# Kernel tuning notes

Hardware: AMD Instinct MI355X
Metric: run time of the kernel (lower is better)

## Reference

```python
import jax, jax.numpy as jnp
import numpy as np

B, N, HIDDEN, IN_DIM = 4, 1024, 64, 6


def setup_inputs() -> dict:
    key = jax.random.key(0)
    ks = jax.random.split(key, 8)
    pos = jax.random.normal(ks[0], (B, N, 3), dtype=jnp.float32)
    vel = jax.random.normal(ks[1], (B, N, 3), dtype=jnp.float32)
    # edge MLP params (Linear stores W as [out,in] in torch; we use [in,out])
    s1 = 1.0 / np.sqrt(IN_DIM)
    s2 = 1.0 / np.sqrt(HIDDEN)
    W1 = jax.random.uniform(ks[2], (IN_DIM, HIDDEN), jnp.float32, -s1, s1)
    b1 = jax.random.uniform(ks[3], (HIDDEN,), jnp.float32, -s1, s1)
    W2 = jax.random.uniform(ks[4], (HIDDEN, HIDDEN), jnp.float32, -s2, s2)
    b2 = jax.random.uniform(ks[5], (HIDDEN,), jnp.float32, -s2, s2)
    W3 = jax.random.uniform(ks[6], (HIDDEN, 3), jnp.float32, -s2, s2)
    b3 = jax.random.uniform(ks[7], (3,), jnp.float32, -s2, s2)
    return {"pos": pos, "vel": vel, "W1": W1, "b1": b1, "W2": W2, "b2": b2, "W3": W3, "b3": b3}


def reference(pos, vel, W1, b1, W2, b2, W3, b3):
    # all-pairs differences: r_ij[b,i,j] = pos[b,j] - pos[b,i]   [B,N,N,3]
    r_ij = pos[:, None, :, :] - pos[:, :, None, :]
    v_ij = vel[:, None, :, :] - vel[:, :, None, :]
    edge_inputs = jnp.concatenate([r_ij, v_ij], axis=-1)  # [B,N,N,6]
    h = jax.nn.relu(jnp.einsum('bijk,kh->bijh', edge_inputs, W1) + b1)
    h = jax.nn.relu(jnp.einsum('bijh,hg->bijg', h, W2) + b2)
    f_ij = jnp.einsum('bijg,go->bijo', h, W3) + b3  # [B,N,N,3]
    # antisymmetrize over (i,j); diagonal becomes exactly 0
    f_sym = (f_ij - jnp.swapaxes(f_ij, 1, 2)) * 0.5
    acc = jnp.sum(f_sym, axis=2)  # [B,N,3]
    return acc
```

## Files before the change

### kernel.cpp

```cpp
#include <hip/hip_runtime.h>

#define NB   4
#define NPTS 1024
#define HID  64
#define NU   1056

typedef float f32x4 __attribute__((ext_vector_type(4)));
typedef float f32x2 __attribute__((ext_vector_type(2)));
typedef short bf16x8 __attribute__((ext_vector_type(8)));
typedef unsigned int u32;
typedef unsigned short u16;

__device__ inline u16 f2bf(float x) {
    union { float f; unsigned u; } v; v.f = x;
    return (u16)((v.u + 0x7FFFu + ((v.u >> 16) & 1u)) >> 16);
}
__device__ inline u32 cvt_pk_bf16(float lo, float hi) {
    u32 r; asm("v_cvt_pk_bf16_f32 %0, %1, %2" : "=v"(r) : "v"(lo), "v"(hi)); return r;
}
__device__ inline u32 pk_relu2(u32 a) {
    u32 r; asm("v_pk_max_i16 %0, %1, 0" : "=v"(r) : "v"(a)); return r;
}

__global__ __launch_bounds__(256) void precompute(
    const float* __restrict__ pos, const float* __restrict__ vel,
    const float* __restrict__ W1, const float* __restrict__ W2,
    float* __restrict__ P, u16* __restrict__ W2T) {
    if (blockIdx.x == NB * NPTS / 4) {
        for (int e = threadIdx.x; e < HID * HID; e += 256) {
            const int ch = e >> 6, k = e & 63;
            W2T[e] = f2bf(W2[k * HID + ch]);
        }
        return;
    }
    const int t   = blockIdx.x * 256 + threadIdx.x;
    const int row = t >> 6;
    const int k   = t & 63;
    const float* pp = pos + row * 3;
    const float* vv = vel + row * 3;
    float acc = 0.f;
    #pragma unroll
    for (int c = 0; c < 3; ++c) acc = fmaf(pp[c], W1[c * HID + k], acc);
    #pragma unroll
    for (int c = 0; c < 3; ++c) acc = fmaf(vv[c], W1[(3 + c) * HID + k], acc);
    P[row * HID + k] = acc;
}

__device__ inline void emit_tile(const f32x4 Ht[4], float sgn, int rowbase,
                                 const float* __restrict__ W3,
                                 float* __restrict__ F, int c, int g) {
    #pragma unroll
    for (int r = 0; r < 4; ++r) {
        float f0 = 0.f, f1 = 0.f, f2 = 0.f;
        #pragma unroll
        for (int n = 0; n < 4; ++n) {
            const int ch = n * 16 + c;
            const float h = Ht[n][r];
            f0 = fmaf(h, W3[ch * 3 + 0], f0);
            f1 = fmaf(h, W3[ch * 3 + 1], f1);
            f2 = fmaf(h, W3[ch * 3 + 2], f2);
        }
        #pragma unroll
        for (int off = 1; off < 16; off <<= 1) {
            f0 += __shfl_xor(f0, off, 64);
            f1 += __shfl_xor(f1, off, 64);
            f2 += __shfl_xor(f2, off, 64);
        }
        if (c < 3) {
            const float v = (c == 0) ? f0 : ((c == 1) ? f1 : f2);
            atomicAdd(&F[(size_t)(rowbase + g * 4 + r) * 3 + c], sgn * v);
        }
    }
}

__device__ inline void do_jt(const f32x2* __restrict__ pj2,
                             const f32x2* __restrict__ bb2,
                             const f32x2* __restrict__ pi2,
                             const bf16x8* __restrict__ BfL,
                             const float* __restrict__ b2v,
                             bool accHj, f32x4* __restrict__ Hj,
                             float* __restrict__ qout) {
    union { bf16x8 v; u32 u[4]; } ap[2], am[2];
    #pragma unroll
    for (int kk = 0; kk < 2; ++kk)
        #pragma unroll
        for (int d = 0; d < 4; ++d) {
            f32x2 u  = pi2[kk * 4 + d] - pj2[kk * 4 + d];
            f32x2 tp = bb2[kk * 4 + d] - u;
            f32x2 tm = bb2[kk * 4 + d] + u;
            ap[kk].u[d] = pk_relu2(cvt_pk_bf16(tp.x, tp.y));
            am[kk].u[d] = pk_relu2(cvt_pk_bf16(tm.x, tm.y));
        }
    const f32x2 z2 = {0.f, 0.f};
    #pragma unroll
    for (int n = 0; n < 4; ++n) {
        const bf16x8 B0 = BfL[n * 64];
        const bf16x8 B1 = BfL[(4 + n) * 64];
        const f32x4 Ci = {b2v[n], b2v[n], b2v[n], b2v[n]};
        f32x4 Cp = __builtin_amdgcn_mfma_f32_16x16x32_bf16(ap[0].v, B0, Ci, 0, 0, 0);
        Cp       = __builtin_amdgcn_mfma_f32_16x16x32_bf16(ap[1].v, B1, Cp, 0, 0, 0);
        f32x4 Cm = __builtin_amdgcn_mfma_f32_16x16x32_bf16(am[0].v, B0, Ci, 0, 0, 0);
        Cm       = __builtin_amdgcn_mfma_f32_16x16x32_bf16(am[1].v, B1, Cm, 0, 0, 0);
        f32x2 cp01 = {Cp[0], Cp[1]}, cp23 = {Cp[2], Cp[3]};
        f32x2 cm01 = {Cm[0], Cm[1]}, cm23 = {Cm[2], Cm[3]};
        f32x2 d01 = __builtin_elementwise_max(cp01, z2) -
                    __builtin_elementwise_max(cm01, z2);
        f32x2 d23 = __builtin_elementwise_max(cp23, z2) -
                    __builtin_elementwise_max(cm23, z2);
        if (accHj) {
            f32x4 dd4 = {d01.x, d01.y, d23.x, d23.y};
            Hj[n] += dd4;
        }
        f32x2 q = d01 + d23;
        qout[n] = q.x + q.y;
    }
}

__global__ __launch_bounds__(128, 2) void inet_pair(
    const float* __restrict__ P,  const float* __restrict__ b1,
    const u16* __restrict__ W2T,  const float* __restrict__ b2,
    const float* __restrict__ W3, float* __restrict__ F) {
    __shared__ __align__(16) u16 sBf[512 * 8];

    const int tid = threadIdx.x;
    for (int s = tid; s < 512; s += 128) {
        const int f = s >> 6, l = s & 63;
        const int n = f & 3, kk = f >> 2, cc = l & 15, gg = l >> 4;
        ((uint4*)sBf)[s] = *(const uint4*)(W2T + (size_t)(n * 16 + cc) * HID + kk * 32 + gg * 8);
    }
    __syncthreads();

    const int lane = tid & 63;
    const int c    = lane & 15;
    const int g    = lane >> 4;
    const bf16x8* BfL = ((const bf16x8*)sBf) + lane;

    const int unit = blockIdx.x * 2 + (tid >> 6);
    const int b    = unit / NU;
    const int u    = unit - b * NU;
    int m = (int)((sqrtf((float)(4 * u + 1)) - 1.0f) * 0.5f);
    while (m * (m + 1) > u) --m;
    while ((m + 1) * (m + 2) <= u) ++m;
    const int I  = u - m * (m + 1);
    const int J0 = 2 * m, J1 = 2 * m + 1;
    const bool jt0act = (I != J1);
    const bool diag0  = (I == J0);
    const bool diag1  = (I == J1);

    const float* Pb   = P + (size_t)b * NPTS * HID;
    const int    koff = g * 8;

    union V4 { f32x4 v; f32x2 p[2]; };

    f32x2 bb2[8], pj0[8], pj1[8];
    {
        V4 v0, v1, v2, v3;
        v0.v = *(const f32x4*)(b1 + koff);
        v1.v = *(const f32x4*)(b1 + koff + 4);
        v2.v = *(const f32x4*)(b1 + koff + 32);
        v3.v = *(const f32x4*)(b1 + koff + 36);
        bb2[0] = v0.p[0]; bb2[1] = v0.p[1]; bb2[2] = v1.p[0]; bb2[3] = v1.p[1];
        bb2[4] = v2.p[0]; bb2[5] = v2.p[1]; bb2[6] = v3.p[0]; bb2[7] = v3.p[1];
    }
    {
        const float* base = Pb + (size_t)(J0 * 16 + c) * HID + koff;
        V4 v0, v1, v2, v3;
        v0.v = *(const f32x4*)(base);
        v1.v = *(const f32x4*)(base + 4);
        v2.v = *(const f32x4*)(base + 32);
        v3.v = *(const f32x4*)(base + 36);
        pj0[0] = v0.p[0]; pj0[1] = v0.p[1]; pj0[2] = v1.p[0]; pj0[3] = v1.p[1];
        pj0[4] = v2.p[0]; pj0[5] = v2.p[1]; pj0[6] = v3.p[0]; pj0[7] = v3.p[1];
    }
    {
        const float* base = Pb + (size_t)(J1 * 16 + c) * HID + koff;
        V4 v0, v1, v2, v3;
        v0.v = *(const f32x4*)(base);
        v1.v = *(const f32x4*)(base + 4);
        v2.v = *(const f32x4*)(base + 32);
        v3.v = *(const f32x4*)(base + 36);
        pj1[0] = v0.p[0]; pj1[1] = v0.p[1]; pj1[2] = v1.p[0]; pj1[3] = v1.p[1];
        pj1[4] = v2.p[0]; pj1[5] = v2.p[1]; pj1[6] = v3.p[0]; pj1[7] = v3.p[1];
    }
    float b2v[4];
    #pragma unroll
    for (int n = 0; n < 4; ++n) b2v[n] = b2[n * 16 + c];

    f32x4 Hi[4], Hj0[4], Hj1[4];
    #pragma unroll
    for (int n = 0; n < 4; ++n) {
        Hi[n]  = (f32x4){0.f, 0.f, 0.f, 0.f};
        Hj0[n] = (f32x4){0.f, 0.f, 0.f, 0.f};
        Hj1[n] = (f32x4){0.f, 0.f, 0.f, 0.f};
    }

    const float* Pi0 = Pb + (size_t)(I * 16) * HID + koff;

    for (int i1 = 0; i1 < 4; ++i1) {
        const float selm = (g == i1) ? 1.0f : 0.0f;
        #pragma unroll
        for (int i2 = 0; i2 < 4; ++i2) {
            const float* pib = Pi0 + (size_t)(i1 * 4 + i2) * HID;
            V4 w0, w1, w2, w3;
            w0.v = *(const f32x4*)(pib);
            w1.v = *(const f32x4*)(pib + 4);
            w2.v = *(const f32x4*)(pib + 32);
            w3.v = *(const f32x4*)(pib + 36);
            f32x2 pi2[8];
            pi2[0] = w0.p[0]; pi2[1] = w0.p[1]; pi2[2] = w1.p[0]; pi2[3] = w1.p[1];
            pi2[4] = w2.p[0]; pi2[5] = w2.p[1]; pi2[6] = w3.p[0]; pi2[7] = w3.p[1];

            float q0[4], q1[4];
            if (jt0act) {
                do_jt(pj0, bb2, pi2, BfL, b2v, !diag0, Hj0, q0);
            } else {
                q0[0] = q0[1] = q0[2] = q0[3] = 0.f;
            }
            do_jt(pj1, bb2, pi2, BfL, b2v, !diag1, Hj1, q1);

            #pragma unroll
            for (int n = 0; n < 4; ++n) {
                float s = q0[n] + q1[n];
                s += __shfl_xor(s, 16, 64);
                s += __shfl_xor(s, 32, 64);
                Hi[n][i2] = fmaf(selm, s, Hi[n][i2]);
            }
        }
    }

    const int rowbase = b * NPTS;
    emit_tile(Hi, 0.5f, rowbase + I * 16, W3, F, c, g);
    if (jt0act && !diag0)
        emit_tile(Hj0, -0.5f, rowbase + J0 * 16, W3, F, c, g);
    if (!diag1)
        emit_tile(Hj1, -0.5f, rowbase + J1 * 16, W3, F, c, g);
}

extern "C" void kernel_launch(void* const* d_in, const int* in_sizes, int n_in,
                              void* d_out, int out_size, void* d_ws, size_t ws_size,
                              hipStream_t stream) {
    const float* pos = (const float*)d_in[0];
    const float* vel = (const float*)d_in[1];
    const float* W1  = (const float*)d_in[2];
    const float* b1  = (const float*)d_in[3];
    const float* W2  = (const float*)d_in[4];
    const float* b2  = (const float*)d_in[5];
    const float* W3  = (const float*)d_in[6];
    const float* b3  = (const float*)d_in[7];
    (void)b3;
    float* out = (float*)d_out;
    float* P   = (float*)d_ws;
    u16*   W2T = (u16*)((char*)d_ws + (size_t)NB * NPTS * HID * 4);

    hipMemsetAsync(out, 0, (size_t)out_size * sizeof(float), stream);
    precompute<<<dim3(NB * NPTS / 4 + 1), dim3(256), 0, stream>>>(pos, vel, W1, W2, P, W2T);
    inet_pair<<<dim3(NB * NU / 2), dim3(128), 0, stream>>>(P, b1, W2T, b2, W3, out);
}
```

Before: 101.9 us.

## Split each pair unit's output channels across two waves per block

Each block now handles one pair-tile unit instead of two, and its two waves each take half of the 64 hidden output channels (two of four 16-channel groups). This halves per-wave MFMA and accumulator work and register use and doubles the grid, aiming for more parallelism and latency hiding. In exchange, both waves redo the same layer-1 activation build and P loads, and atomic adds per output row double because each half emits partial sums.

```diff
diff --git a/kernel.cpp b/kernel.cpp
--- a/kernel.cpp
+++ b/kernel.cpp
@@ -46,15 +46,15 @@
     P[row * HID + k] = acc;
 }
 
-__device__ inline void emit_tile(const f32x4 Ht[4], float sgn, int rowbase,
-                                 const float* __restrict__ W3,
+__device__ inline void emit_half(const f32x4 Ht[2], float sgn, int rowbase,
+                                 int nbase, const float* __restrict__ W3,
                                  float* __restrict__ F, int c, int g) {
     #pragma unroll
     for (int r = 0; r < 4; ++r) {
         float f0 = 0.f, f1 = 0.f, f2 = 0.f;
         #pragma unroll
-        for (int n = 0; n < 4; ++n) {
-            const int ch = n * 16 + c;
+        for (int n = 0; n < 2; ++n) {
+            const int ch = (nbase + n) * 16 + c;
             const float h = Ht[n][r];
             f0 = fmaf(h, W3[ch * 3 + 0], f0);
             f1 = fmaf(h, W3[ch * 3 + 1], f1);
@@ -77,7 +77,7 @@
                              const f32x2* __restrict__ bb2,
                              const f32x2* __restrict__ pi2,
                              const bf16x8* __restrict__ BfL,
-                             const float* __restrict__ b2v,
+                             const float* __restrict__ b2v, int nbase,
                              bool accHj, f32x4* __restrict__ Hj,
                              float* __restrict__ qout) {
     union { bf16x8 v; u32 u[4]; } ap[2], am[2];
@@ -93,10 +93,10 @@
         }
     const f32x2 z2 = {0.f, 0.f};
     #pragma unroll
-    for (int n = 0; n < 4; ++n) {
-        const bf16x8 B0 = BfL[n * 64];
-        const bf16x8 B1 = BfL[(4 + n) * 64];
-        const f32x4 Ci = {b2v[n], b2v[n], b2v[n], b2v[n]};
+    for (int nn = 0; nn < 2; ++nn) {
+        const bf16x8 B0 = BfL[(nbase + nn) * 64];
+        const bf16x8 B1 = BfL[(4 + nbase + nn) * 64];
+        const f32x4 Ci = {b2v[nn], b2v[nn], b2v[nn], b2v[nn]};
         f32x4 Cp = __builtin_amdgcn_mfma_f32_16x16x32_bf16(ap[0].v, B0, Ci, 0, 0, 0);
         Cp       = __builtin_amdgcn_mfma_f32_16x16x32_bf16(ap[1].v, B1, Cp, 0, 0, 0);
         f32x4 Cm = __builtin_amdgcn_mfma_f32_16x16x32_bf16(am[0].v, B0, Ci, 0, 0, 0);
@@ -109,10 +109,10 @@
                     __builtin_elementwise_max(cm23, z2);
         if (accHj) {
             f32x4 dd4 = {d01.x, d01.y, d23.x, d23.y};
-            Hj[n] += dd4;
+            Hj[nn] += dd4;
         }
         f32x2 q = d01 + d23;
-        qout[n] = q.x + q.y;
+        qout[nn] = q.x + q.y;
     }
 }
 
@@ -133,11 +133,13 @@
     const int lane = tid & 63;
     const int c    = lane & 15;
     const int g    = lane >> 4;
+    const int h    = tid >> 6;
+    const int nbase = 2 * h;
     const bf16x8* BfL = ((const bf16x8*)sBf) + lane;
 
-    const int unit = blockIdx.x * 2 + (tid >> 6);
-    const int b    = unit / NU;
-    const int u    = unit - b * NU;
+    const int bu = blockIdx.x;
+    const int b  = bu / NU;
+    const int u  = bu - b * NU;
     int m = (int)((sqrtf((float)(4 * u + 1)) - 1.0f) * 0.5f);
     while (m * (m + 1) > u) --m;
     while ((m + 1) * (m + 2) <= u) ++m;
@@ -182,16 +184,16 @@
         pj1[0] = v0.p[0]; pj1[1] = v0.p[1]; pj1[2] = v1.p[0]; pj1[3] = v1.p[1];
         pj1[4] = v2.p[0]; pj1[5] = v2.p[1]; pj1[6] = v3.p[0]; pj1[7] = v3.p[1];
     }
-    float b2v[4];
-    #pragma unroll
-    for (int n = 0; n < 4; ++n) b2v[n] = b2[n * 16 + c];
-
-    f32x4 Hi[4], Hj0[4], Hj1[4];
-    #pragma unroll
-    for (int n = 0; n < 4; ++n) {
-        Hi[n]  = (f32x4){0.f, 0.f, 0.f, 0.f};
-        Hj0[n] = (f32x4){0.f, 0.f, 0.f, 0.f};
-        Hj1[n] = (f32x4){0.f, 0.f, 0.f, 0.f};
+    float b2v[2];
+    #pragma unroll
+    for (int nn = 0; nn < 2; ++nn) b2v[nn] = b2[(nbase + nn) * 16 + c];
+
+    f32x4 Hi[2], Hj0[2], Hj1[2];
+    #pragma unroll
+    for (int nn = 0; nn < 2; ++nn) {
+        Hi[nn]  = (f32x4){0.f, 0.f, 0.f, 0.f};
+        Hj0[nn] = (f32x4){0.f, 0.f, 0.f, 0.f};
+        Hj1[nn] = (f32x4){0.f, 0.f, 0.f, 0.f};
     }
 
     const float* Pi0 = Pb + (size_t)(I * 16) * HID + koff;
@@ -210,30 +212,30 @@
             pi2[0] = w0.p[0]; pi2[1] = w0.p[1]; pi2[2] = w1.p[0]; pi2[3] = w1.p[1];
             pi2[4] = w2.p[0]; pi2[5] = w2.p[1]; pi2[6] = w3.p[0]; pi2[7] = w3.p[1];
 
-            float q0[4], q1[4];
+            float q0[2], q1[2];
             if (jt0act) {
-                do_jt(pj0, bb2, pi2, BfL, b2v, !diag0, Hj0, q0);
+                do_jt(pj0, bb2, pi2, BfL, b2v, nbase, !diag0, Hj0, q0);
             } else {
-                q0[0] = q0[1] = q0[2] = q0[3] = 0.f;
+                q0[0] = q0[1] = 0.f;
             }
-            do_jt(pj1, bb2, pi2, BfL, b2v, !diag1, Hj1, q1);
+            do_jt(pj1, bb2, pi2, BfL, b2v, nbase, !diag1, Hj1, q1);
 
             #pragma unroll
-            for (int n = 0; n < 4; ++n) {
-                float s = q0[n] + q1[n];
+            for (int nn = 0; nn < 2; ++nn) {
+                float s = q0[nn] + q1[nn];
                 s += __shfl_xor(s, 16, 64);
                 s += __shfl_xor(s, 32, 64);
-                Hi[n][i2] = fmaf(selm, s, Hi[n][i2]);
+                Hi[nn][i2] = fmaf(selm, s, Hi[nn][i2]);
             }
         }
     }
 
     const int rowbase = b * NPTS;
-    emit_tile(Hi, 0.5f, rowbase + I * 16, W3, F, c, g);
+    emit_half(Hi, 0.5f, rowbase + I * 16, nbase, W3, F, c, g);
     if (jt0act && !diag0)
-        emit_tile(Hj0, -0.5f, rowbase + J0 * 16, W3, F, c, g);
+        emit_half(Hj0, -0.5f, rowbase + J0 * 16, nbase, W3, F, c, g);
     if (!diag1)
-        emit_tile(Hj1, -0.5f, rowbase + J1 * 16, W3, F, c, g);
+        emit_half(Hj1, -0.5f, rowbase + J1 * 16, nbase, W3, F, c, g);
 }
 
 extern "C" void kernel_launch(void* const* d_in, const int* in_sizes, int n_in,
@@ -254,5 +256,5 @@
 
     hipMemsetAsync(out, 0, (size_t)out_size * sizeof(float), stream);
     precompute<<<dim3(NB * NPTS / 4 + 1), dim3(256), 0, stream>>>(pos, vel, W1, W2, P, W2T);
-    inet_pair<<<dim3(NB * NU / 2), dim3(128), 0, stream>>>(P, b1, W2T, b2, W3, out);
-}
+    inet_pair<<<dim3(NB * NU), dim3(128), 0, stream>>>(P, b1, W2T, b2, W3, out);
+}
```

Result: slower. 127.0 us (+24.6%).
